# Kernel tuning notes

Measured on AMD Instinct MI355X. Metric: run time of the kernel, lower is better.

Reference implementation:

```python
import jax, jax.numpy as jnp
import numpy as np

H, DH = 8, 64  # num_heads, head_dim


def setup_inputs() -> dict:
    key = jax.random.key(0)
    ks = jax.random.split(key, 7)
    m, nq, nkv, d = 4, 2048, 2048, 512
    return {
        "xq": jax.random.normal(ks[0], (m, nq, d), jnp.float32),
        "xk": jax.random.normal(ks[1], (m, nkv, d), jnp.float32),
        "xv": jax.random.normal(ks[2], (m, nkv, d), jnp.float32),
        "Wq": jax.random.normal(ks[3], (d, H * DH), jnp.float32) * 0.02,
        "Wk": jax.random.normal(ks[4], (d, H * DH), jnp.float32) * 0.02,
        "Wv": jax.random.normal(ks[5], (d, H * DH), jnp.float32) * 0.02,
        "Wo": jax.random.normal(ks[6], (H * DH, d), jnp.float32) * 0.02,
        "bo": jnp.zeros((d,), jnp.float32),
    }


def _split_heads(t):
    # [b, n, h*d] -> [b, h, n, d]
    b, n, _ = t.shape
    return t.reshape(b, n, H, DH).transpose(0, 2, 1, 3)


def reference(xq, xk, xv, Wq, Wk, Wv, Wo, bo):
    scale = DH ** -0.5
    q = _split_heads(xq @ Wq)   # [b,h,nq,dh]
    k = _split_heads(xk @ Wk)   # [b,h,nkv,dh]
    v = _split_heads(xv @ Wv)   # [b,h,nkv,dh]
    dots = jnp.einsum("bhqd,bhkd->bhqk", q, k) * scale  # [b,h,nq,nkv]
    # diagonal attention term: query attends to its own (k,v) projection
    xq_k = _split_heads(xq @ Wk)
    xq_v = _split_heads(xq @ Wv)
    diag = jnp.sum(q * xq_k, axis=-1, keepdims=True) * scale  # [b,h,nq,1]
    dots = jnp.concatenate([dots, diag], axis=-1)  # [b,h,nq,nkv+1]
    attn = jax.nn.softmax(dots, axis=-1)
    out = jnp.einsum("bhqk,bhkd->bhqd", attn[..., :-1], v) + attn[..., -1:] * xq_v
    b, _, nq, _ = out.shape
    out = out.transpose(0, 2, 1, 3).reshape(b, nq, H * DH)  # merge heads
    return out @ Wo + bo
```

## Files before the change

### kernel.cpp

```cpp
#include <hip/hip_runtime.h>

#define LOG2E 1.44269504088896f
#define CS (0.125f * LOG2E)

typedef __bf16 bf16x8 __attribute__((ext_vector_type(8)));
typedef float f32x4 __attribute__((ext_vector_type(4)));
typedef unsigned short u16x8 __attribute__((ext_vector_type(8)));

#if __has_builtin(__builtin_amdgcn_exp2f)
#define fexp2(x) __builtin_amdgcn_exp2f(x)
#else
extern "C" __device__ float __ocml_native_exp2_f32(float);
#define fexp2(x) __ocml_native_exp2_f32(x)
#endif

__device__ __forceinline__ unsigned short f2bf(float f) {
  union { float f; unsigned int u; } v{f};
  unsigned int r = v.u + 0x7fffu + ((v.u >> 16) & 1u);
  return (unsigned short)(r >> 16);
}
__device__ __forceinline__ float bf2f(unsigned short u) {
  union { unsigned int u; float f; } v; v.u = ((unsigned int)u) << 16; return v.f;
}
__device__ __forceinline__ unsigned int pkr(float a, float b) {
  unsigned int ua = __builtin_bit_cast(unsigned int, a) + 0x8000u;
  unsigned int ub = __builtin_bit_cast(unsigned int, b) + 0x8000u;
  return __builtin_amdgcn_perm(ub, ua, 0x07060302);
}

typedef __attribute__((address_space(3))) unsigned int lds32_t;
typedef const __attribute__((address_space(1))) unsigned int glb32_t;
__device__ __forceinline__ void gld16(const unsigned short* g, unsigned short* l) {
  __builtin_amdgcn_global_load_lds((glb32_t*)(unsigned long long)g,
                                   (lds32_t*)(unsigned int)(unsigned long long)l,
                                   16, 0, 0);
}

__global__ __launch_bounds__(256) void conv_all(
    const float* __restrict__ xq, const float* __restrict__ xk, const float* __restrict__ xv,
    const float* __restrict__ Wq, const float* __restrict__ Wk,
    const float* __restrict__ Wv, const float* __restrict__ Wo,
    unsigned short* __restrict__ oxq, unsigned short* __restrict__ oxk, unsigned short* __restrict__ oxv,
    unsigned short* __restrict__ oWq, unsigned short* __restrict__ oWk,
    unsigned short* __restrict__ oWv, unsigned short* __restrict__ oWo) {
  __shared__ unsigned short T[64 * 65];
  const int blk = blockIdx.x;
  if (blk < 12288) {
    const int N4 = (8192 * 512) / 4;
    int idx = blk * 256 + threadIdx.x;
    const float* src; unsigned short* dst; int i;
    if (idx < N4)          { src = xq; dst = oxq; i = idx; }
    else if (idx < 2 * N4) { src = xk; dst = oxk; i = idx - N4; }
    else                   { src = xv; dst = oxv; i = idx - 2 * N4; }
    float4 v = ((const float4*)src)[i];
    ushort4 o; o.x = f2bf(v.x); o.y = f2bf(v.y); o.z = f2bf(v.z); o.w = f2bf(v.w);
    ((ushort4*)dst)[i] = o;
  } else {
    const int wblk = blk - 12288;
    const int wsel = wblk >> 6;
    const int tile = wblk & 63;
    const int tk = (tile >> 3) * 64, tn = (tile & 7) * 64;
    const float* src = (wsel == 0) ? Wq : (wsel == 1) ? Wk : (wsel == 2) ? Wv : Wo;
    unsigned short* dst = (wsel == 0) ? oWq : (wsel == 1) ? oWk : (wsel == 2) ? oWv : oWo;
    const float scale = (wsel == 0) ? CS : 1.0f;
    const int rr = threadIdx.x >> 4;
    const int cc = (threadIdx.x & 15) * 4;
#pragma unroll
    for (int i = 0; i < 4; i++) {
      int row = rr + i * 16;
      float4 v = *(const float4*)&src[(size_t)(tk + row) * 512 + tn + cc];
      T[(cc + 0) * 65 + row] = f2bf(v.x * scale);
      T[(cc + 1) * 65 + row] = f2bf(v.y * scale);
      T[(cc + 2) * 65 + row] = f2bf(v.z * scale);
      T[(cc + 3) * 65 + row] = f2bf(v.w * scale);
    }
    __syncthreads();
#pragma unroll
    for (int i = 0; i < 4; i++) {
      int n = rr + i * 16;
      ushort4 o;
      o.x = T[n * 65 + cc + 0]; o.y = T[n * 65 + cc + 1];
      o.z = T[n * 65 + cc + 2]; o.w = T[n * 65 + cc + 3];
      *(ushort4*)&dst[(size_t)(tn + n) * 512 + tk + cc] = o;
    }
  }
}

__device__ __forceinline__ void gemm_tile(
    const unsigned short* __restrict__ A, const unsigned short* __restrict__ Bt,
    int rowBlk, int colBlk, unsigned short* As, unsigned short* Bs, f32x4 (&acc)[4][4]) {
  const int t = threadIdx.x;
  const int lane = t & 63, c = lane & 15, g = lane >> 4;
  const int w = t >> 6;
  const int wm = w & 1, wn = w >> 1;
#pragma unroll
  for (int i = 0; i < 4; i++)
#pragma unroll
    for (int j = 0; j < 4; j++)
#pragma unroll
      for (int r = 0; r < 4; r++) acc[i][j][r] = 0.f;

  for (int kk = 0; kk < 512; kk += 32) {
    __syncthreads();
#pragma unroll
    for (int i = 0; i < 2; i++) {
      int idx = t + 256 * i;
      int r = idx >> 2, ch = idx & 3;
      gld16(&A[(size_t)(rowBlk + r) * 512 + kk + ch * 8], &As[idx * 8]);
      gld16(&Bt[(size_t)(colBlk + r) * 512 + kk + ch * 8], &Bs[idx * 8]);
    }
    __syncthreads();
    bf16x8 af[4], bfr[4];
#pragma unroll
    for (int i = 0; i < 4; i++)
      af[i] = __builtin_bit_cast(bf16x8, *(const u16x8*)&As[(wm * 64 + i * 16 + c) * 32 + g * 8]);
#pragma unroll
    for (int j = 0; j < 4; j++)
      bfr[j] = __builtin_bit_cast(bf16x8, *(const u16x8*)&Bs[(wn * 64 + j * 16 + c) * 32 + g * 8]);
#pragma unroll
    for (int i = 0; i < 4; i++)
#pragma unroll
      for (int j = 0; j < 4; j++)
        acc[i][j] = __builtin_amdgcn_mfma_f32_16x16x32_bf16(af[i], bfr[j], acc[i][j], 0, 0, 0);
  }
}

__global__ __launch_bounds__(256) void proj_all(
    const unsigned short* __restrict__ xq, const unsigned short* __restrict__ xk,
    const unsigned short* __restrict__ xv,
    const unsigned short* __restrict__ Wq, const unsigned short* __restrict__ Wk,
    const unsigned short* __restrict__ Wv,
    unsigned short* __restrict__ Qo, unsigned short* __restrict__ XKo,
    unsigned short* __restrict__ XVo, unsigned short* __restrict__ Ko,
    unsigned short* __restrict__ Vto) {
  __shared__ unsigned short As[128 * 32];
  __shared__ unsigned short Bs[128 * 32];
  const int rowBlk = blockIdx.x * 128;
  const int y = blockIdx.y;
  const unsigned short* A; const unsigned short* Bt; int colBlk; int mode;
  unsigned short* out;
  if (y < 12) {
    int wsel = y >> 2;
    A = xq; colBlk = (y & 3) * 128; mode = 0;
    Bt = (wsel == 0) ? Wq : (wsel == 1) ? Wk : Wv;
    out = (wsel == 0) ? Qo : (wsel == 1) ? XKo : XVo;
  } else if (y < 16) {
    A = xk; Bt = Wk; out = Ko; colBlk = (y - 12) * 128; mode = 0;
  } else {
    A = xv; Bt = Wv; out = Vto; colBlk = (y - 16) * 128; mode = 1;
  }
  f32x4 acc[4][4];
  gemm_tile(A, Bt, rowBlk, colBlk, As, Bs, acc);
  const int t = threadIdx.x;
  const int w = t >> 6, lane = t & 63, c = lane & 15, g = lane >> 4;
  const int wm = w & 1, wn = w >> 1;
  if (mode == 0) {
#pragma unroll
    for (int i = 0; i < 4; i++)
#pragma unroll
      for (int j = 0; j < 4; j++)
#pragma unroll
        for (int r = 0; r < 4; r++) {
          int row = rowBlk + wm * 64 + i * 16 + g * 4 + r;
          int col = colBlk + wn * 64 + j * 16 + c;
          out[(size_t)row * 512 + col] = f2bf(acc[i][j][r]);
        }
  } else {
#pragma unroll
    for (int i = 0; i < 4; i++) {
      int tok0 = rowBlk + wm * 64 + i * 16 + g * 4;
      int bb = tok0 >> 11, n0 = tok0 & 2047;
#pragma unroll
      for (int j = 0; j < 4; j++) {
        int col = colBlk + wn * 64 + j * 16 + c;
        int hh = col >> 6, dh = col & 63;
        ushort4 o;
        o.x = f2bf(acc[i][j][0]); o.y = f2bf(acc[i][j][1]);
        o.z = f2bf(acc[i][j][2]); o.w = f2bf(acc[i][j][3]);
        *(ushort4*)&out[((size_t)(bb * 8 + hh) * 64 + dh) * 2048 + n0] = o;
      }
    }
  }
}

__global__ __launch_bounds__(256) void gemm_out(
    const unsigned short* __restrict__ A, const unsigned short* __restrict__ Bt,
    float* __restrict__ out, const float* __restrict__ bias) {
  __shared__ unsigned short As[128 * 32];
  __shared__ unsigned short Bs[64 * 32];
  const int rowBlk = blockIdx.x * 128;
  const int colBlk = blockIdx.y * 64;
  const int t = threadIdx.x;
  const int lane = t & 63, c = lane & 15, g = lane >> 4;
  const int w = t >> 6;
  const int wm = w & 1, wn = w >> 1;
  f32x4 acc[4][2];
#pragma unroll
  for (int i = 0; i < 4; i++)
#pragma unroll
    for (int j = 0; j < 2; j++)
#pragma unroll
      for (int r = 0; r < 4; r++) acc[i][j][r] = 0.f;

  for (int kk = 0; kk < 512; kk += 32) {
    __syncthreads();
#pragma unroll
    for (int i = 0; i < 2; i++) {
      int idx = t + 256 * i;
      int r = idx >> 2, ch = idx & 3;
      gld16(&A[(size_t)(rowBlk + r) * 512 + kk + ch * 8], &As[idx * 8]);
    }
    {
      int r = t >> 2, ch = t & 3;
      gld16(&Bt[(size_t)(colBlk + r) * 512 + kk + ch * 8], &Bs[t * 8]);
    }
    __syncthreads();
    bf16x8 af[4], bfr[2];
#pragma unroll
    for (int i = 0; i < 4; i++)
      af[i] = __builtin_bit_cast(bf16x8, *(const u16x8*)&As[(wm * 64 + i * 16 + c) * 32 + g * 8]);
#pragma unroll
    for (int j = 0; j < 2; j++)
      bfr[j] = __builtin_bit_cast(bf16x8, *(const u16x8*)&Bs[(wn * 32 + j * 16 + c) * 32 + g * 8]);
#pragma unroll
    for (int i = 0; i < 4; i++)
#pragma unroll
      for (int j = 0; j < 2; j++)
        acc[i][j] = __builtin_amdgcn_mfma_f32_16x16x32_bf16(af[i], bfr[j], acc[i][j], 0, 0, 0);
  }
#pragma unroll
  for (int i = 0; i < 4; i++)
#pragma unroll
    for (int j = 0; j < 2; j++)
#pragma unroll
      for (int r = 0; r < 4; r++) {
        int row = rowBlk + wm * 64 + i * 16 + g * 4 + r;
        int col = colBlk + wn * 32 + j * 16 + c;
        out[(size_t)row * 512 + col] = acc[i][j][r] + bias[col];
      }
}

__global__ __launch_bounds__(512, 4) void attn_kernel(
    const unsigned short* __restrict__ Q, const unsigned short* __restrict__ K,
    const unsigned short* __restrict__ Vt, const unsigned short* __restrict__ XK,
    const unsigned short* __restrict__ XV, unsigned short* __restrict__ O) {
  __shared__ unsigned short Ks[2][64 * 64];
  __shared__ unsigned short Vs[2][64 * 64];
  __shared__ unsigned short Ps[8][16 * 72];
  __shared__ float Scr[8][32];
  const int t = threadIdx.x;
  const int w = t >> 6, lane = t & 63, c = lane & 15, g = lane >> 4;
  const int qt = blockIdx.x, h = blockIdx.y, b = blockIdx.z;
  const size_t hb = (size_t)b * (2048 * 512) + h * 64;
  const size_t vhb = (size_t)(b * 8 + h) * 64 * 2048;
  const int qbase = qt * 128 + w * 16;
  unsigned short* Pw = &Ps[w][0];

  const int sr = t >> 3, sch = t & 7;
  const int ssl = (sch ^ (sr & 7)) * 8;
  const size_t kgoff = hb + (size_t)sr * 512 + ssl;
  const size_t vgoff = vhb + (size_t)sr * 2048 + ssl;

  const int sw0 = ((g ^ (c & 7)) << 3);
  const int sw1 = (((g | 4) ^ (c & 7)) << 3);

  bf16x8 qf[2];
#pragma unroll
  for (int hf = 0; hf < 2; hf++)
    qf[hf] = __builtin_bit_cast(bf16x8,
        *(const u16x8*)&Q[hb + (size_t)(qbase + c) * 512 + hf * 32 + g * 8]);

  f32x4 accO[4];
  float lq = 0.f;
#pragma unroll
  for (int jd = 0; jd < 4; jd++)
#pragma unroll
    for (int r = 0; r < 4; r++) accO[jd][r] = 0.f;

  gld16(&K[kgoff], &Ks[0][t * 8]);
  gld16(&Vt[vgoff], &Vs[0][t * 8]);
  __syncthreads();

  int cur = 0;
  for (int kt = 0; kt < 32; kt++) {
    if (kt < 31) {
      gld16(&K[kgoff + (size_t)(kt + 1) * (64 * 512)], &Ks[cur ^ 1][t * 8]);
      gld16(&Vt[vgoff + (size_t)(kt + 1) * 64], &Vs[cur ^ 1][t * 8]);
    }
    const unsigned short* Kc = &Ks[cur][0];
    const unsigned short* Vc = &Vs[cur][0];

    f32x4 s[4];
    __builtin_amdgcn_s_setprio(1);
#pragma unroll
    for (int j = 0; j < 4; j++) {
      bf16x8 kf0 = __builtin_bit_cast(bf16x8, *(const u16x8*)&Kc[(j * 16 + c) * 64 + sw0]);
      bf16x8 kf1 = __builtin_bit_cast(bf16x8, *(const u16x8*)&Kc[(j * 16 + c) * 64 + sw1]);
      f32x4 z; z[0] = z[1] = z[2] = z[3] = 0.f;
      z = __builtin_amdgcn_mfma_f32_16x16x32_bf16(kf0, qf[0], z, 0, 0, 0);
      z = __builtin_amdgcn_mfma_f32_16x16x32_bf16(kf1, qf[1], z, 0, 0, 0);
      s[j] = z;
    }
    __builtin_amdgcn_s_setprio(0);

    float sum = 0.f;
#pragma unroll
    for (int j = 0; j < 4; j++) {
      float p0 = fexp2(s[j][0]);
      float p1 = fexp2(s[j][1]);
      float p2 = fexp2(s[j][2]);
      float p3 = fexp2(s[j][3]);
      sum += (p0 + p1) + (p2 + p3);
      uint2 pw; pw.x = pkr(p0, p1); pw.y = pkr(p2, p3);
      *(uint2*)&Pw[c * 72 + j * 16 + g * 4] = pw;
    }
    lq += sum;

    bf16x8 pf0 = __builtin_bit_cast(bf16x8, *(const u16x8*)&Pw[c * 72 + g * 8]);
    bf16x8 pf1 = __builtin_bit_cast(bf16x8, *(const u16x8*)&Pw[c * 72 + 32 + g * 8]);
    __builtin_amdgcn_s_setprio(1);
#pragma unroll
    for (int jd = 0; jd < 4; jd++) {
      bf16x8 v0 = __builtin_bit_cast(bf16x8, *(const u16x8*)&Vc[(jd * 16 + c) * 64 + sw0]);
      bf16x8 v1 = __builtin_bit_cast(bf16x8, *(const u16x8*)&Vc[(jd * 16 + c) * 64 + sw1]);
      accO[jd] = __builtin_amdgcn_mfma_f32_16x16x32_bf16(pf0, v0, accO[jd], 0, 0, 0);
      accO[jd] = __builtin_amdgcn_mfma_f32_16x16x32_bf16(pf1, v1, accO[jd], 0, 0, 0);
    }
    __builtin_amdgcn_s_setprio(0);

    if (kt < 31) __syncthreads();
    cur ^= 1;
  }

  lq += __shfl_xor(lq, 16);
  lq += __shfl_xor(lq, 32);

  {
    const int qc = qbase + c;
    float part = 0.f;
    {
      const unsigned short* qp = &Q[hb + (size_t)qc * 512 + g * 16];
      const unsigned short* xp = &XK[hb + (size_t)qc * 512 + g * 16];
      u16x8 q0 = *(const u16x8*)&qp[0], q1 = *(const u16x8*)&qp[8];
      u16x8 x0 = *(const u16x8*)&xp[0], x1 = *(const u16x8*)&xp[8];
#pragma unroll
      for (int ii = 0; ii < 8; ii++)
        part += bf2f(q0[ii]) * bf2f(x0[ii]) + bf2f(q1[ii]) * bf2f(x1[ii]);
    }
    part += __shfl_xor(part, 16);
    part += __shfl_xor(part, 32);
    float pd = fexp2(part);
    float inv = 1.f / (lq + pd);
    if (g == 0) {
      Scr[w][c] = inv;
      Scr[w][16 + c] = pd * inv;
    }
    __builtin_amdgcn_s_waitcnt(0);
    f32x4 a4 = *(const f32x4*)&Scr[w][g * 4];
    f32x4 p4 = *(const f32x4*)&Scr[w][16 + g * 4];
#pragma unroll
    for (int jd = 0; jd < 4; jd++)
#pragma unroll
      for (int r = 0; r < 4; r++) {
        int qr = qbase + g * 4 + r;
        float xv = bf2f(XV[hb + (size_t)qr * 512 + jd * 16 + c]);
        float val = accO[jd][r] * a4[r] + p4[r] * xv;
        O[((size_t)(b * 2048 + qr)) * 512 + h * 64 + jd * 16 + c] = f2bf(val);
      }
  }
}

extern "C" void kernel_launch(void* const* d_in, const int* in_sizes, int n_in,
                              void* d_out, int out_size, void* d_ws, size_t ws_size,
                              hipStream_t stream) {
  const float* xq = (const float*)d_in[0];
  const float* xk = (const float*)d_in[1];
  const float* xv = (const float*)d_in[2];
  const float* Wq = (const float*)d_in[3];
  const float* Wk = (const float*)d_in[4];
  const float* Wv = (const float*)d_in[5];
  const float* Wo = (const float*)d_in[6];
  const float* bo = (const float*)d_in[7];

  unsigned short* ws = (unsigned short*)d_ws;
  const size_t MD = 8192ull * 512;
  const size_t WD = 512ull * 512;
  unsigned short* xq_b = ws;
  unsigned short* xk_b = xq_b + MD;
  unsigned short* xv_b = xk_b + MD;
  unsigned short* Wq_t = xv_b + MD;
  unsigned short* Wk_t = Wq_t + WD;
  unsigned short* Wv_t = Wk_t + WD;
  unsigned short* Wo_t = Wv_t + WD;
  unsigned short* Qb  = Wo_t + WD;
  unsigned short* Kb  = Qb + MD;
  unsigned short* Vtb = Kb + MD;
  unsigned short* XKb = Vtb + MD;
  unsigned short* XVb = XKb + MD;
  unsigned short* Ob  = XVb + MD;

  conv_all<<<dim3(12544), 256, 0, stream>>>(xq, xk, xv, Wq, Wk, Wv, Wo,
                                            xq_b, xk_b, xv_b, Wq_t, Wk_t, Wv_t, Wo_t);
  proj_all<<<dim3(64, 20), 256, 0, stream>>>(xq_b, xk_b, xv_b, Wq_t, Wk_t, Wv_t,
                                             Qb, XKb, XVb, Kb, Vtb);
  attn_kernel<<<dim3(16, 8, 4), 512, 0, stream>>>(Qb, Kb, Vtb, XKb, XVb, Ob);
  gemm_out<<<dim3(64, 8), 256, 0, stream>>>(Ob, Wo_t, (float*)d_out, bo);
}
```

Before: 205.9 us.

## Software-pipeline attention loop: overlap QK^T of next tile with PV of previous

Restructures the attention main loop into a skewed pipeline. Each iteration computes the QK^T scores for tile kt while running the PV MFMAs for tile kt-1, with a prologue and an epilogue added around the loop. P is double-buffered per warp and V is triple-buffered in shared memory so the exp/softmax stage can overlap with the matrix-core work. This adds LDS footprint and register pressure, which could reduce occupancy under the 512x4 launch bounds.

Result: faster. 201.6 us (-2.1%).

```diff
diff --git a/kernel.cpp b/kernel.cpp
--- a/kernel.cpp
+++ b/kernel.cpp
@@ -245,8 +245,8 @@
     const unsigned short* __restrict__ Vt, const unsigned short* __restrict__ XK,
     const unsigned short* __restrict__ XV, unsigned short* __restrict__ O) {
   __shared__ unsigned short Ks[2][64 * 64];
-  __shared__ unsigned short Vs[2][64 * 64];
-  __shared__ unsigned short Ps[8][16 * 72];
+  __shared__ unsigned short Vs[3][64 * 64];
+  __shared__ unsigned short Ps[2][8][16 * 72];
   __shared__ float Scr[8][32];
   const int t = threadIdx.x;
   const int w = t >> 6, lane = t & 63, c = lane & 15, g = lane >> 4;
@@ -254,7 +254,6 @@
   const size_t hb = (size_t)b * (2048 * 512) + h * 64;
   const size_t vhb = (size_t)(b * 8 + h) * 64 * 2048;
   const int qbase = qt * 128 + w * 16;
-  unsigned short* Pw = &Ps[w][0];
 
   const int sr = t >> 3, sch = t & 7;
   const int ssl = (sch ^ (sr & 7)) * 8;
@@ -281,28 +280,22 @@
   gld16(&Vt[vgoff], &Vs[0][t * 8]);
   __syncthreads();
 
-  int cur = 0;
-  for (int kt = 0; kt < 32; kt++) {
-    if (kt < 31) {
-      gld16(&K[kgoff + (size_t)(kt + 1) * (64 * 512)], &Ks[cur ^ 1][t * 8]);
-      gld16(&Vt[vgoff + (size_t)(kt + 1) * 64], &Vs[cur ^ 1][t * 8]);
-    }
-    const unsigned short* Kc = &Ks[cur][0];
-    const unsigned short* Vc = &Vs[cur][0];
-
+  gld16(&K[kgoff + (size_t)(64 * 512)], &Ks[1][t * 8]);
+  gld16(&Vt[vgoff + 64], &Vs[1][t * 8]);
+  {
+    unsigned short* Pw = &Ps[0][w][0];
     f32x4 s[4];
     __builtin_amdgcn_s_setprio(1);
 #pragma unroll
     for (int j = 0; j < 4; j++) {
-      bf16x8 kf0 = __builtin_bit_cast(bf16x8, *(const u16x8*)&Kc[(j * 16 + c) * 64 + sw0]);
-      bf16x8 kf1 = __builtin_bit_cast(bf16x8, *(const u16x8*)&Kc[(j * 16 + c) * 64 + sw1]);
+      bf16x8 kf0 = __builtin_bit_cast(bf16x8, *(const u16x8*)&Ks[0][(j * 16 + c) * 64 + sw0]);
+      bf16x8 kf1 = __builtin_bit_cast(bf16x8, *(const u16x8*)&Ks[0][(j * 16 + c) * 64 + sw1]);
       f32x4 z; z[0] = z[1] = z[2] = z[3] = 0.f;
       z = __builtin_amdgcn_mfma_f32_16x16x32_bf16(kf0, qf[0], z, 0, 0, 0);
       z = __builtin_amdgcn_mfma_f32_16x16x32_bf16(kf1, qf[1], z, 0, 0, 0);
       s[j] = z;
     }
     __builtin_amdgcn_s_setprio(0);
-
     float sum = 0.f;
 #pragma unroll
     for (int j = 0; j < 4; j++) {
@@ -315,10 +308,32 @@
       *(uint2*)&Pw[c * 72 + j * 16 + g * 4] = pw;
     }
     lq += sum;
-
-    bf16x8 pf0 = __builtin_bit_cast(bf16x8, *(const u16x8*)&Pw[c * 72 + g * 8]);
-    bf16x8 pf1 = __builtin_bit_cast(bf16x8, *(const u16x8*)&Pw[c * 72 + 32 + g * 8]);
+  }
+  __syncthreads();
+
+  int vprev = 0, vcur = 1, vnext = 2;
+  for (int kt = 1; kt < 32; kt++) {
+    if (kt < 31) {
+      gld16(&K[kgoff + (size_t)(kt + 1) * (64 * 512)], &Ks[(kt + 1) & 1][t * 8]);
+      gld16(&Vt[vgoff + (size_t)(kt + 1) * 64], &Vs[vnext][t * 8]);
+    }
+    const unsigned short* Pp = &Ps[(kt - 1) & 1][w][0];
+    bf16x8 pf0 = __builtin_bit_cast(bf16x8, *(const u16x8*)&Pp[c * 72 + g * 8]);
+    bf16x8 pf1 = __builtin_bit_cast(bf16x8, *(const u16x8*)&Pp[c * 72 + 32 + g * 8]);
+
+    const unsigned short* Kc = &Ks[kt & 1][0];
+    f32x4 s[4];
     __builtin_amdgcn_s_setprio(1);
+#pragma unroll
+    for (int j = 0; j < 4; j++) {
+      bf16x8 kf0 = __builtin_bit_cast(bf16x8, *(const u16x8*)&Kc[(j * 16 + c) * 64 + sw0]);
+      bf16x8 kf1 = __builtin_bit_cast(bf16x8, *(const u16x8*)&Kc[(j * 16 + c) * 64 + sw1]);
+      f32x4 z; z[0] = z[1] = z[2] = z[3] = 0.f;
+      z = __builtin_amdgcn_mfma_f32_16x16x32_bf16(kf0, qf[0], z, 0, 0, 0);
+      z = __builtin_amdgcn_mfma_f32_16x16x32_bf16(kf1, qf[1], z, 0, 0, 0);
+      s[j] = z;
+    }
+    const unsigned short* Vc = &Vs[vprev][0];
 #pragma unroll
     for (int jd = 0; jd < 4; jd++) {
       bf16x8 v0 = __builtin_bit_cast(bf16x8, *(const u16x8*)&Vc[(jd * 16 + c) * 64 + sw0]);
@@ -328,8 +343,40 @@
     }
     __builtin_amdgcn_s_setprio(0);
 
+    {
+      unsigned short* Pw = &Ps[kt & 1][w][0];
+      float sum = 0.f;
+#pragma unroll
+      for (int j = 0; j < 4; j++) {
+        float p0 = fexp2(s[j][0]);
+        float p1 = fexp2(s[j][1]);
+        float p2 = fexp2(s[j][2]);
+        float p3 = fexp2(s[j][3]);
+        sum += (p0 + p1) + (p2 + p3);
+        uint2 pw; pw.x = pkr(p0, p1); pw.y = pkr(p2, p3);
+        *(uint2*)&Pw[c * 72 + j * 16 + g * 4] = pw;
+      }
+      lq += sum;
+    }
+
     if (kt < 31) __syncthreads();
-    cur ^= 1;
+    int tmp = vprev; vprev = vcur; vcur = vnext; vnext = tmp;
+  }
+
+  {
+    const unsigned short* Pp = &Ps[1][w][0];
+    bf16x8 pf0 = __builtin_bit_cast(bf16x8, *(const u16x8*)&Pp[c * 72 + g * 8]);
+    bf16x8 pf1 = __builtin_bit_cast(bf16x8, *(const u16x8*)&Pp[c * 72 + 32 + g * 8]);
+    const unsigned short* Vc = &Vs[vprev][0];
+    __builtin_amdgcn_s_setprio(1);
+#pragma unroll
+    for (int jd = 0; jd < 4; jd++) {
+      bf16x8 v0 = __builtin_bit_cast(bf16x8, *(const u16x8*)&Vc[(jd * 16 + c) * 64 + sw0]);
+      bf16x8 v1 = __builtin_bit_cast(bf16x8, *(const u16x8*)&Vc[(jd * 16 + c) * 64 + sw1]);
+      accO[jd] = __builtin_amdgcn_mfma_f32_16x16x32_bf16(pf0, v0, accO[jd], 0, 0, 0);
+      accO[jd] = __builtin_amdgcn_mfma_f32_16x16x32_bf16(pf1, v1, accO[jd], 0, 0, 0);
+    }
+    __builtin_amdgcn_s_setprio(0);
   }
 
   lq += __shfl_xor(lq, 16);
```
